# Kernel optimization log

Measured on AMD Instinct MI355X. Metric: run time of the kernel, lower is better.

## Reference

```python
import jax, jax.numpy as jnp
import numpy as np

N_QUBITS = 8
N_WORDS = 16
DEGREE = 3
N_ANSATZ_LAYERS = 2
VOCAB = 50257
EMB = 512
BATCH = 16
N_ROTS = 4 * N_QUBITS * N_ANSATZ_LAYERS  # 64
DIM = 2 ** N_QUBITS


def _ry_mat(th):
    # [[cos, -sin],[sin, cos]] on theta/2, batched over leading dim
    c = jnp.cos(th / 2).astype(jnp.complex64)
    s = jnp.sin(th / 2).astype(jnp.complex64)
    return jnp.stack([jnp.stack([c, -s], -1), jnp.stack([s, c], -1)], -2)


def _rx_mat(th):
    # [[cos, -i sin],[-i sin, cos]] on theta/2
    c = jnp.cos(th / 2).astype(jnp.complex64)
    s = jnp.sin(th / 2).astype(jnp.complex64)
    return jnp.stack([jnp.stack([c, -1j * s], -1), jnp.stack([-1j * s, c], -1)], -2)


def _apply_1q(st, M, w):
    # st: [BB, 2^n] complex, M: [BB,2,2]; wire 0 is the most-significant axis (tq convention)
    BB = st.shape[0]
    s = st.reshape(BB, 2 ** w, 2, -1)
    s = jnp.einsum('bij,bljr->blir', M, s)
    return s.reshape(BB, -1)


def _apply_ctrl(st, M, c, t, n):
    # controlled-1q gate: apply M on target t only in the control=1 subspace
    BB = st.shape[0]
    full = st.reshape((BB,) + (2,) * n)
    s0 = jnp.take(full, 0, axis=c + 1)
    s1 = jnp.take(full, 1, axis=c + 1)
    ta = (t if t < c else t - 1) + 1  # target axis after removing control axis
    s1 = jnp.moveaxis(s1, ta, -1)
    s1 = jnp.einsum('bij,b...j->b...i', M, s1)
    s1 = jnp.moveaxis(s1, -1, ta)
    return jnp.stack([s0, s1], axis=c + 1).reshape(BB, -1)


def _sim14(st, params, n, layers):
    # circuit-14 ansatz: ry ring, crx down-ring, ry ring, crx up-ring (per layer)
    idx = 0
    for _ in range(layers):
        for i in range(n):
            st = _apply_1q(st, _ry_mat(params[:, idx]), i); idx += 1
        for i in range(n - 1, -1, -1):
            st = _apply_ctrl(st, _rx_mat(params[:, idx]), i, (i + 1) % n, n); idx += 1
        for i in range(n):
            st = _apply_1q(st, _ry_mat(params[:, idx]), i); idx += 1
        for i in [n - 1] + list(range(n - 1)):
            st = _apply_ctrl(st, _rx_mat(params[:, idx]), i, (i - 1) % n, n); idx += 1
    return st


def _apply_unitaries(base, wparams, coeffs):
    # base: [B, DIM]; wparams: [B, W, N_ROTS]; coeffs: [B, W] complex -> LCU sum_w c_w U_w |psi>
    B, W = wparams.shape[0], wparams.shape[1]
    rep = jnp.repeat(base, W, axis=0)  # matches torch repeat(1,W).view(-1,DIM)
    st = _sim14(rep, wparams.reshape(B * W, -1), N_QUBITS, N_ANSATZ_LAYERS)
    return jnp.einsum('bwi,bw->bi', st.reshape(B, W, DIM), coeffs)


def _measure_xyz(st, n):
    # Pauli X/Y/Z expectations per wire; order: [x_0..x_{n-1}, y_..., z_...]
    BB = st.shape[0]
    xs, ys, zs = [], [], []
    for w in range(n):
        s = st.reshape(BB, 2 ** w, 2, -1)
        a0, a1 = s[:, :, 0, :], s[:, :, 1, :]
        cross = jnp.sum(jnp.conj(a0) * a1, axis=(1, 2))
        xs.append(2 * jnp.real(cross))
        ys.append(2 * jnp.imag(cross))
        zs.append(jnp.sum(jnp.abs(a0) ** 2 - jnp.abs(a1) ** 2, axis=(1, 2)))
    return jnp.concatenate([jnp.stack(xs, -1), jnp.stack(ys, -1), jnp.stack(zs, -1)], axis=-1)


def reference(x, embedding_W, emb2rot_W, emb2rot_b, poly_coeffs, mix_coeffs_ri, qff_params, ff1_W, ff1_b, ff2_W, ff2_b):
    B = x.shape[0]
    mix = (mix_coeffs_ri[:, 0] + 1j * mix_coeffs_ri[:, 1]).astype(jnp.complex64)
    coeffs = mix / jnp.maximum(jnp.sum(jnp.abs(mix)), 1e-12)  # L1 normalize
    coeffs = jnp.broadcast_to(coeffs[None, :], (B, N_WORDS))
    emb = embedding_W[x]                       # [B, W, EMB]
    wparams = emb @ emb2rot_W.T + emb2rot_b    # [B, W, N_ROTS]; dropout is identity in eval
    base = jnp.zeros((B, DIM), jnp.complex64).at[:, 0].set(1.0)
    acc = poly_coeffs[0] * base
    work = base
    for d in range(1, DEGREE + 1):
        work = _apply_unitaries(work, wparams, coeffs)
        acc = acc + poly_coeffs[d] * work
    mixed = acc / jnp.sum(jnp.abs(poly_coeffs))
    final_probs = jnp.linalg.norm(mixed, axis=-1)
    normed = mixed / jnp.maximum(final_probs, 1e-12)[:, None]
    qp = jnp.broadcast_to(qff_params[None, :4 * N_QUBITS], (B, 4 * N_QUBITS))  # qff uses 1 layer
    st = _sim14(normed, qp, N_QUBITS, 1)
    exps = _measure_xyz(st, N_QUBITS)          # [B, 3*n_qubits]
    h = jax.nn.relu(exps @ ff1_W.T + ff1_b)
    op = h @ ff2_W.T + ff2_b
    return op, jnp.mean(final_probs)


def setup_inputs():
    key = jax.random.key(0)
    ks = jax.random.split(key, 12)
    x = jax.random.randint(ks[0], (BATCH, N_WORDS), 0, VOCAB)
    embedding_W = jax.random.normal(ks[1], (VOCAB, EMB), jnp.float32) * 0.02
    emb2rot_W = jax.random.normal(ks[2], (N_ROTS, EMB), jnp.float32) * (1.0 / np.sqrt(EMB))
    emb2rot_b = jax.random.normal(ks[3], (N_ROTS,), jnp.float32) * 0.01
    poly_coeffs = jax.random.uniform(ks[4], (DEGREE + 1,), jnp.float32)
    mix_coeffs_ri = jax.random.uniform(ks[5], (N_WORDS, 2), jnp.float32)
    qff_params = jax.random.uniform(ks[6], (N_ROTS,), jnp.float32)
    NM = 3 * N_QUBITS
    ff1_W = jax.random.normal(ks[7], (EMB, NM), jnp.float32) * (1.0 / np.sqrt(NM))
    ff1_b = jnp.zeros((EMB,), jnp.float32)
    ff2_W = jax.random.normal(ks[8], (VOCAB, EMB), jnp.float32) * (1.0 / np.sqrt(EMB))
    ff2_b = jnp.zeros((VOCAB,), jnp.float32)
    return {"x": x, "embedding_W": embedding_W, "emb2rot_W": emb2rot_W, "emb2rot_b": emb2rot_b,
            "poly_coeffs": poly_coeffs, "mix_coeffs_ri": mix_coeffs_ri, "qff_params": qff_params,
            "ff1_W": ff1_W, "ff1_b": ff1_b, "ff2_W": ff2_W, "ff2_b": ff2_b}
```

## Files before the change

### kernel.cpp

```cpp
#include <hip/hip_runtime.h>
#include <hip/hip_bf16.h>

#define NQ 8
#define DIM 256
#define NB 16
#define NW 16
#define VOCABN 50257
#define EMBN 512

__device__ __forceinline__ float2 shfl2(float2 a, int m){
  float2 r; r.x = __shfl_xor(a.x, m, 64); r.y = __shfl_xor(a.y, m, 64); return r;
}
__device__ __forceinline__ float wave_sum(float x){
  #pragma unroll
  for (int off = 1; off < 64; off <<= 1) x += __shfl_xor(x, off, 64);
  return x;
}

__device__ __forceinline__ void ry_pair(float2& a0, float2& a1, float c, float s){
  float2 n0 = make_float2(c*a0.x - s*a1.x, c*a0.y - s*a1.y);
  float2 n1 = make_float2(s*a0.x + c*a1.x, s*a0.y + c*a1.y);
  a0 = n0; a1 = n1;
}
__device__ __forceinline__ void rx_pair(float2& a0, float2& a1, float c, float s){
  float2 n0 = make_float2(c*a0.x + s*a1.y, c*a0.y - s*a1.x);
  float2 n1 = make_float2(c*a1.x + s*a0.y, c*a1.y - s*a0.x);
  a0 = n0; a1 = n1;
}

__device__ __forceinline__ void apply_gate(float2 v[4], int lane, int kind, int cbit, int tbit,
                                           float c, float s){
  if (kind == 0){
    if (tbit == 7){ ry_pair(v[0], v[2], c, s); ry_pair(v[1], v[3], c, s); }
    else if (tbit == 6){ ry_pair(v[0], v[1], c, s); ry_pair(v[2], v[3], c, s); }
    else {
      int m = 1 << tbit;
      #pragma unroll
      for (int r = 0; r < 4; ++r){
        float2 w = shfl2(v[r], m);
        float sg = (lane & m) ? s : -s;
        v[r] = make_float2(c*v[r].x + sg*w.x, c*v[r].y + sg*w.y);
      }
    }
  } else {
    if (tbit >= 6){
      if (cbit >= 6){
        if (cbit == 7) rx_pair(v[2], v[3], c, s);
        else           rx_pair(v[1], v[3], c, s);
      } else {
        int cm = 1 << cbit;
        if (lane & cm){
          if (tbit == 7){ rx_pair(v[0], v[2], c, s); rx_pair(v[1], v[3], c, s); }
          else          { rx_pair(v[0], v[1], c, s); rx_pair(v[2], v[3], c, s); }
        }
      }
    } else {
      int m = 1 << tbit;
      if (cbit >= 6){
        int r0 = (cbit == 6) ? 1 : 2;
        float2 w0 = shfl2(v[r0], m);
        float2 w1 = shfl2(v[3], m);
        v[r0] = make_float2(c*v[r0].x + s*w0.y, c*v[r0].y - s*w0.x);
        v[3]  = make_float2(c*v[3].x  + s*w1.y, c*v[3].y  - s*w1.x);
      } else {
        int cm = 1 << cbit;
        bool act = (lane & cm) != 0;
        #pragma unroll
        for (int r = 0; r < 4; ++r){
          float2 w = shfl2(v[r], m);
          if (act) v[r] = make_float2(c*v[r].x + s*w.y, c*v[r].y - s*w.x);
        }
      }
    }
  }
}

__device__ __forceinline__ void sim32(float2 v[4], int lane, const float2* __restrict__ cs){
  constexpr int KIND[32] = {0,0,0,0,0,0,0,0, 1,1,1,1,1,1,1,1, 0,0,0,0,0,0,0,0, 1,1,1,1,1,1,1,1};
  constexpr int CB[32]   = {0,0,0,0,0,0,0,0, 0,1,2,3,4,5,6,7, 0,0,0,0,0,0,0,0, 0,7,6,5,4,3,2,1};
  constexpr int TB[32]   = {7,6,5,4,3,2,1,0, 7,0,1,2,3,4,5,6, 7,6,5,4,3,2,1,0, 1,0,7,6,5,4,3,2};
  #pragma unroll
  for (int g = 0; g < 32; ++g){
    float2 p = cs[g];
    apply_gate(v, lane, KIND[g], CB[g], TB[g], p.x, p.y);
  }
}

__device__ __forceinline__ void measure_xyz(const float2 v[4], int lane, float* exps){
  #pragma unroll
  for (int q = 0; q < 8; ++q){
    const int t = 7 - q;
    float xr = 0.f, xi = 0.f, zz = 0.f;
    if (t == 7){
      #pragma unroll
      for (int r = 0; r < 2; ++r){
        float2 a0 = v[r], a1 = v[r+2];
        xr += a0.x*a1.x + a0.y*a1.y;
        xi += a0.x*a1.y - a0.y*a1.x;
        zz += (a0.x*a0.x + a0.y*a0.y) - (a1.x*a1.x + a1.y*a1.y);
      }
    } else if (t == 6){
      #pragma unroll
      for (int r = 0; r < 4; r += 2){
        float2 a0 = v[r], a1 = v[r+1];
        xr += a0.x*a1.x + a0.y*a1.y;
        xi += a0.x*a1.y - a0.y*a1.x;
        zz += (a0.x*a0.x + a0.y*a0.y) - (a1.x*a1.x + a1.y*a1.y);
      }
    } else {
      int m = 1 << t;
      #pragma unroll
      for (int r = 0; r < 4; ++r){
        float2 a = v[r];
        float2 w = shfl2(a, m);
        if (!(lane & m)){
          xr += a.x*w.x + a.y*w.y;
          xi += a.x*w.y - a.y*w.x;
          zz += (a.x*a.x + a.y*a.y) - (w.x*w.x + w.y*w.y);
        }
      }
    }
    xr = wave_sum(xr); xi = wave_sum(xi); zz = wave_sum(zz);
    if (lane == 0){ exps[q] = 2.f*xr; exps[8+q] = 2.f*xi; exps[16+q] = zz; }
  }
}

__global__ __launch_bounds__(64) void k_prep(
    const int* __restrict__ x, const float* __restrict__ embW,
    const float* __restrict__ e2rW, const float* __restrict__ e2rb,
    const float* __restrict__ mixri, const float* __restrict__ qff,
    float* __restrict__ wcs, float* __restrict__ coeffs, float* __restrict__ qcs)
{
  const int p = blockIdx.x;
  const int j = threadIdx.x;
  const int tok = x[p];
  const float4* er = (const float4*)(embW + (size_t)tok * EMBN);
  const float4* wr = (const float4*)(e2rW + (size_t)j * EMBN);
  float acc = e2rb[j];
  #pragma unroll 4
  for (int k = 0; k < EMBN/4; ++k){
    float4 e = er[k], w4 = wr[k];
    acc += e.x*w4.x + e.y*w4.y + e.z*w4.z + e.w*w4.w;
  }
  float th = 0.5f * acc;
  wcs[(p*64 + j)*2 + 0] = cosf(th);
  wcs[(p*64 + j)*2 + 1] = sinf(th);
  if (p == 0){
    if (j < 32){ float t = 0.5f * qff[j]; qcs[2*j] = cosf(t); qcs[2*j+1] = sinf(t); }
    if (j < 16){
      float ssum = 0.f;
      for (int i = 0; i < 16; ++i){
        float mr = mixri[2*i], mi = mixri[2*i+1];
        ssum += sqrtf(mr*mr + mi*mi);
      }
      ssum = fmaxf(ssum, 1e-12f);
      coeffs[2*j]   = mixri[2*j]   / ssum;
      coeffs[2*j+1] = mixri[2*j+1] / ssum;
    }
  }
}

__global__ __launch_bounds__(1024) void k_sim(
    const float* __restrict__ wcs, const float* __restrict__ coeffs,
    const float* __restrict__ qcs, const float* __restrict__ poly,
    const float* __restrict__ ff1W, const float* __restrict__ ff1b,
    float* __restrict__ hT, float* __restrict__ fprobs)
{
  const int b = blockIdx.x;
  const int tid = threadIdx.x;
  const int w = tid >> 6;
  const int lane = tid & 63;

  __shared__ float2 stall[NW][DIM];
  __shared__ float2 partial[4][DIM];
  __shared__ float2 work[DIM];
  __shared__ float2 accs[DIM];
  __shared__ float exps[24];

  if (tid < DIM){
    float p0 = poly[0];
    float one = (tid == 0) ? 1.f : 0.f;
    work[tid] = make_float2(one, 0.f);
    accs[tid] = make_float2(p0*one, 0.f);
  }
  __syncthreads();

  const float2 coef = make_float2(coeffs[2*w], coeffs[2*w+1]);
  const float2* mycs = ((const float2*)wcs) + (b*NW + w)*64;

  for (int d = 1; d <= 3; ++d){
    float2 v[4];
    #pragma unroll
    for (int r = 0; r < 4; ++r) v[r] = work[(r<<6) | lane];
    for (int l = 0; l < 2; ++l) sim32(v, lane, mycs + 32*l);
    #pragma unroll
    for (int r = 0; r < 4; ++r){
      float2 a = v[r];
      stall[w][(r<<6) | lane] = make_float2(coef.x*a.x - coef.y*a.y, coef.x*a.y + coef.y*a.x);
    }
    __syncthreads();
    {
      int idx = tid & 255, grp = tid >> 8;
      float2 s = make_float2(0.f, 0.f);
      #pragma unroll
      for (int ww = 0; ww < 4; ++ww){
        float2 a = stall[grp*4 + ww][idx];
        s.x += a.x; s.y += a.y;
      }
      partial[grp][idx] = s;
    }
    __syncthreads();
    if (tid < DIM){
      float2 s = make_float2(0.f, 0.f);
      #pragma unroll
      for (int g2 = 0; g2 < 4; ++g2){ s.x += partial[g2][tid].x; s.y += partial[g2][tid].y; }
      float pd = poly[d];
      work[tid] = s;
      accs[tid].x += pd*s.x; accs[tid].y += pd*s.y;
    }
    __syncthreads();
  }

  const float psum = fabsf(poly[0]) + fabsf(poly[1]) + fabsf(poly[2]) + fabsf(poly[3]);
  if (tid < DIM){
    work[tid] = make_float2(accs[tid].x/psum, accs[tid].y/psum);
  }
  __syncthreads();

  if (w == 0){
    float2 v[4];
    float ss = 0.f;
    #pragma unroll
    for (int r = 0; r < 4; ++r){
      float2 m = work[(r<<6) | lane];
      v[r] = m; ss += m.x*m.x + m.y*m.y;
    }
    ss = wave_sum(ss);
    float fp = sqrtf(ss);
    if (lane == 0) fprobs[b] = fp;
    float inv = 1.f / fmaxf(fp, 1e-12f);
    #pragma unroll
    for (int r = 0; r < 4; ++r){ v[r].x *= inv; v[r].y *= inv; }
    sim32(v, lane, (const float2*)qcs);
    measure_xyz(v, lane, exps);
  }
  __syncthreads();

  if (tid < EMBN){
    float a = ff1b[tid];
    const float* wr = ff1W + tid*24;
    #pragma unroll
    for (int m2 = 0; m2 < 24; ++m2) a += exps[m2]*wr[m2];
    a = fmaxf(a, 0.f);
    hT[tid*NB + b] = a;
  }
}

__global__ __launch_bounds__(256) void k_out(
    const float* __restrict__ hT, const float* __restrict__ ff2W,
    const float* __restrict__ ff2b, const float* __restrict__ fprobs,
    float* __restrict__ out)
{
  const int v = blockIdx.x*256 + threadIdx.x;
  if (blockIdx.x == 0 && threadIdx.x == 0){
    float s = 0.f;
    #pragma unroll
    for (int i = 0; i < 16; ++i) s += fprobs[i];
    out[(size_t)NB*VOCABN] = s * (1.f/16.f);
  }
  if (v >= VOCABN) return;
  const float4* wr = (const float4*)(ff2W + (size_t)v * EMBN);
  float acc[16];
  #pragma unroll
  for (int i = 0; i < 16; ++i) acc[i] = 0.f;
  for (int kc = 0; kc < EMBN/4; ++kc){
    float4 w4 = wr[kc];
    const float* hk = hT + kc*64;
    #pragma unroll
    for (int i = 0; i < 16; ++i)
      acc[i] += w4.x*hk[i] + w4.y*hk[16+i] + w4.z*hk[32+i] + w4.w*hk[48+i];
  }
  float bias = ff2b[v];
  #pragma unroll
  for (int i = 0; i < 16; ++i) out[(size_t)i*VOCABN + v] = acc[i] + bias;
}

extern "C" void kernel_launch(void* const* d_in, const int* in_sizes, int n_in,
                              void* d_out, int out_size, void* d_ws, size_t ws_size,
                              hipStream_t stream)
{
  const int*   x     = (const int*)  d_in[0];
  const float* embW  = (const float*)d_in[1];
  const float* e2rW  = (const float*)d_in[2];
  const float* e2rb  = (const float*)d_in[3];
  const float* poly  = (const float*)d_in[4];
  const float* mixri = (const float*)d_in[5];
  const float* qff   = (const float*)d_in[6];
  const float* ff1W  = (const float*)d_in[7];
  const float* ff1b  = (const float*)d_in[8];
  const float* ff2W  = (const float*)d_in[9];
  const float* ff2b  = (const float*)d_in[10];
  float* out = (float*)d_out;
  float* ws  = (float*)d_ws;

  float* wcs    = ws;
  float* coeffs = ws + 32768;
  float* qcs    = ws + 32800;
  float* hT     = ws + 32864;
  float* fprobs = ws + 41056;

  k_prep<<<256, 64, 0, stream>>>(x, embW, e2rW, e2rb, mixri, qff, wcs, coeffs, qcs);
  k_sim <<<NB, 1024, 0, stream>>>(wcs, coeffs, qcs, poly, ff1W, ff1b, hT, fprobs);
  k_out <<<(VOCABN + 255)/256, 256, 0, stream>>>(hT, ff2W, ff2b, fprobs, out);
}
```

Baseline: 319.2 us.

## Fuse prep into sim kernel and stage hidden states in LDS for output GEMV

Folds the embedding-to-rotation prep kernel into the simulation kernel, so each wave computes its own cos/sin angles into shared memory and one launch plus its global round trip disappear. The output projection now copies the whole hidden matrix into shared memory and gives each row to two threads, each covering half of K. The halves are combined through shared memory. This trades global/L2 reads of hT for LDS reads and doubles the thread count per row, while the fused prep runs on only 16 blocks.

```diff
diff --git a/kernel.cpp b/kernel.cpp
--- a/kernel.cpp
+++ b/kernel.cpp
@@ -125,44 +125,11 @@
   }
 }
 
-__global__ __launch_bounds__(64) void k_prep(
+__global__ __launch_bounds__(1024) void k_sim(
     const int* __restrict__ x, const float* __restrict__ embW,
     const float* __restrict__ e2rW, const float* __restrict__ e2rb,
     const float* __restrict__ mixri, const float* __restrict__ qff,
-    float* __restrict__ wcs, float* __restrict__ coeffs, float* __restrict__ qcs)
-{
-  const int p = blockIdx.x;
-  const int j = threadIdx.x;
-  const int tok = x[p];
-  const float4* er = (const float4*)(embW + (size_t)tok * EMBN);
-  const float4* wr = (const float4*)(e2rW + (size_t)j * EMBN);
-  float acc = e2rb[j];
-  #pragma unroll 4
-  for (int k = 0; k < EMBN/4; ++k){
-    float4 e = er[k], w4 = wr[k];
-    acc += e.x*w4.x + e.y*w4.y + e.z*w4.z + e.w*w4.w;
-  }
-  float th = 0.5f * acc;
-  wcs[(p*64 + j)*2 + 0] = cosf(th);
-  wcs[(p*64 + j)*2 + 1] = sinf(th);
-  if (p == 0){
-    if (j < 32){ float t = 0.5f * qff[j]; qcs[2*j] = cosf(t); qcs[2*j+1] = sinf(t); }
-    if (j < 16){
-      float ssum = 0.f;
-      for (int i = 0; i < 16; ++i){
-        float mr = mixri[2*i], mi = mixri[2*i+1];
-        ssum += sqrtf(mr*mr + mi*mi);
-      }
-      ssum = fmaxf(ssum, 1e-12f);
-      coeffs[2*j]   = mixri[2*j]   / ssum;
-      coeffs[2*j+1] = mixri[2*j+1] / ssum;
-    }
-  }
-}
-
-__global__ __launch_bounds__(1024) void k_sim(
-    const float* __restrict__ wcs, const float* __restrict__ coeffs,
-    const float* __restrict__ qcs, const float* __restrict__ poly,
+    const float* __restrict__ poly,
     const float* __restrict__ ff1W, const float* __restrict__ ff1b,
     float* __restrict__ hT, float* __restrict__ fprobs)
 {
@@ -171,22 +138,50 @@
   const int w = tid >> 6;
   const int lane = tid & 63;
 
+  __shared__ float2 wcs_s[NW][64];
+  __shared__ float2 qcs_s[32];
+  __shared__ float  ssum_s;
   __shared__ float2 stall[NW][DIM];
   __shared__ float2 partial[4][DIM];
   __shared__ float2 work[DIM];
   __shared__ float2 accs[DIM];
   __shared__ float exps[24];
 
-  if (tid < DIM){
-    float p0 = poly[0];
-    float one = (tid == 0) ? 1.f : 0.f;
-    work[tid] = make_float2(one, 0.f);
-    accs[tid] = make_float2(p0*one, 0.f);
-  }
-  __syncthreads();
-
-  const float2 coef = make_float2(coeffs[2*w], coeffs[2*w+1]);
-  const float2* mycs = ((const float2*)wcs) + (b*NW + w)*64;
+  {
+    const int j = lane;
+    const int tok = x[b*NW + w];
+    const float4* er  = (const float4*)(embW + (size_t)tok * EMBN);
+    const float4* wr4 = (const float4*)(e2rW + (size_t)j * EMBN);
+    float acc = e2rb[j];
+    #pragma unroll 4
+    for (int k = 0; k < EMBN/4; ++k){
+      float4 e = er[k], w4 = wr4[k];
+      acc += e.x*w4.x + e.y*w4.y + e.z*w4.z + e.w*w4.w;
+    }
+    float th = 0.5f * acc;
+    wcs_s[w][j] = make_float2(cosf(th), sinf(th));
+    if (tid < 32){ float t = 0.5f * qff[tid]; qcs_s[tid] = make_float2(cosf(t), sinf(t)); }
+    if (tid == 0){
+      float ssum = 0.f;
+      #pragma unroll
+      for (int i = 0; i < 16; ++i){
+        float mr = mixri[2*i], mi = mixri[2*i+1];
+        ssum += sqrtf(mr*mr + mi*mi);
+      }
+      ssum_s = fmaxf(ssum, 1e-12f);
+    }
+    if (tid < DIM){
+      float p0 = poly[0];
+      float one = (tid == 0) ? 1.f : 0.f;
+      work[tid] = make_float2(one, 0.f);
+      accs[tid] = make_float2(p0*one, 0.f);
+    }
+  }
+  __syncthreads();
+
+  const float inv_ssum = 1.f / ssum_s;
+  const float2 coef = make_float2(mixri[2*w]*inv_ssum, mixri[2*w+1]*inv_ssum);
+  const float2* mycs = &wcs_s[w][0];
 
   for (int d = 1; d <= 3; ++d){
     float2 v[4];
@@ -241,7 +236,7 @@
     float inv = 1.f / fmaxf(fp, 1e-12f);
     #pragma unroll
     for (int r = 0; r < 4; ++r){ v[r].x *= inv; v[r].y *= inv; }
-    sim32(v, lane, (const float2*)qcs);
+    sim32(v, lane, &qcs_s[0]);
     measure_xyz(v, lane, exps);
   }
   __syncthreads();
@@ -261,28 +256,93 @@
     const float* __restrict__ ff2b, const float* __restrict__ fprobs,
     float* __restrict__ out)
 {
-  const int v = blockIdx.x*256 + threadIdx.x;
-  if (blockIdx.x == 0 && threadIdx.x == 0){
+  __shared__ float4 smem[2048];
+  const int tid = threadIdx.x;
+
+  if (blockIdx.x == 0 && tid == 0){
     float s = 0.f;
     #pragma unroll
     for (int i = 0; i < 16; ++i) s += fprobs[i];
     out[(size_t)NB*VOCABN] = s * (1.f/16.f);
   }
-  if (v >= VOCABN) return;
-  const float4* wr = (const float4*)(ff2W + (size_t)v * EMBN);
-  float acc[16];
-  #pragma unroll
-  for (int i = 0; i < 16; ++i) acc[i] = 0.f;
-  for (int kc = 0; kc < EMBN/4; ++kc){
-    float4 w4 = wr[kc];
-    const float* hk = hT + kc*64;
-    #pragma unroll
-    for (int i = 0; i < 16; ++i)
-      acc[i] += w4.x*hk[i] + w4.y*hk[16+i] + w4.z*hk[32+i] + w4.w*hk[48+i];
-  }
-  float bias = ff2b[v];
-  #pragma unroll
-  for (int i = 0; i < 16; ++i) out[(size_t)i*VOCABN + v] = acc[i] + bias;
+
+  {
+    const float4* hT4 = (const float4*)hT;
+    #pragma unroll
+    for (int i = 0; i < 8; ++i) smem[i*256 + tid] = hT4[i*256 + tid];
+  }
+  __syncthreads();
+
+  const int rrow = tid & 127;
+  const int half = tid >> 7;
+  const int row  = blockIdx.x * 128 + rrow;
+  const bool valid = (row < VOCABN);
+
+  float4 a0 = make_float4(0,0,0,0), a1 = a0, a2 = a0, a3 = a0;
+
+  if (valid){
+    const float4* wv = (const float4*)(ff2W + (size_t)row * EMBN) + half*64;
+    const int kbase = half*256;
+    #pragma unroll 8
+    for (int c = 0; c < 64; ++c){
+      float4 wq = wv[c];
+      const int k0 = (kbase + c*4) << 2;
+      float4 h00 = smem[k0+0],  h01 = smem[k0+1],  h02 = smem[k0+2],  h03 = smem[k0+3];
+      float4 h10 = smem[k0+4],  h11 = smem[k0+5],  h12 = smem[k0+6],  h13 = smem[k0+7];
+      float4 h20 = smem[k0+8],  h21 = smem[k0+9],  h22 = smem[k0+10], h23 = smem[k0+11];
+      float4 h30 = smem[k0+12], h31 = smem[k0+13], h32 = smem[k0+14], h33 = smem[k0+15];
+      a0.x += wq.x*h00.x + wq.y*h10.x + wq.z*h20.x + wq.w*h30.x;
+      a0.y += wq.x*h00.y + wq.y*h10.y + wq.z*h20.y + wq.w*h30.y;
+      a0.z += wq.x*h00.z + wq.y*h10.z + wq.z*h20.z + wq.w*h30.z;
+      a0.w += wq.x*h00.w + wq.y*h10.w + wq.z*h20.w + wq.w*h30.w;
+      a1.x += wq.x*h01.x + wq.y*h11.x + wq.z*h21.x + wq.w*h31.x;
+      a1.y += wq.x*h01.y + wq.y*h11.y + wq.z*h21.y + wq.w*h31.y;
+      a1.z += wq.x*h01.z + wq.y*h11.z + wq.z*h21.z + wq.w*h31.z;
+      a1.w += wq.x*h01.w + wq.y*h11.w + wq.z*h21.w + wq.w*h31.w;
+      a2.x += wq.x*h02.x + wq.y*h12.x + wq.z*h22.x + wq.w*h32.x;
+      a2.y += wq.x*h02.y + wq.y*h12.y + wq.z*h22.y + wq.w*h32.y;
+      a2.z += wq.x*h02.z + wq.y*h12.z + wq.z*h22.z + wq.w*h32.z;
+      a2.w += wq.x*h02.w + wq.y*h12.w + wq.z*h22.w + wq.w*h32.w;
+      a3.x += wq.x*h03.x + wq.y*h13.x + wq.z*h23.x + wq.w*h33.x;
+      a3.y += wq.x*h03.y + wq.y*h13.y + wq.z*h23.y + wq.w*h33.y;
+      a3.z += wq.x*h03.z + wq.y*h13.z + wq.z*h23.z + wq.w*h33.z;
+      a3.w += wq.x*h03.w + wq.y*h13.w + wq.z*h23.w + wq.w*h33.w;
+    }
+  }
+  __syncthreads();
+
+  if (half == 1){
+    smem[0*128 + rrow] = a0;
+    smem[1*128 + rrow] = a1;
+    smem[2*128 + rrow] = a2;
+    smem[3*128 + rrow] = a3;
+  }
+  __syncthreads();
+  if (half == 0 && valid){
+    float4 b0 = smem[0*128 + rrow], b1 = smem[1*128 + rrow];
+    float4 b2 = smem[2*128 + rrow], b3 = smem[3*128 + rrow];
+    a0.x += b0.x; a0.y += b0.y; a0.z += b0.z; a0.w += b0.w;
+    a1.x += b1.x; a1.y += b1.y; a1.z += b1.z; a1.w += b1.w;
+    a2.x += b2.x; a2.y += b2.y; a2.z += b2.z; a2.w += b2.w;
+    a3.x += b3.x; a3.y += b3.y; a3.z += b3.z; a3.w += b3.w;
+    const float bias = ff2b[row];
+    out[(size_t) 0*VOCABN + row] = a0.x + bias;
+    out[(size_t) 1*VOCABN + row] = a0.y + bias;
+    out[(size_t) 2*VOCABN + row] = a0.z + bias;
+    out[(size_t) 3*VOCABN + row] = a0.w + bias;
+    out[(size_t) 4*VOCABN + row] = a1.x + bias;
+    out[(size_t) 5*VOCABN + row] = a1.y + bias;
+    out[(size_t) 6*VOCABN + row] = a1.z + bias;
+    out[(size_t) 7*VOCABN + row] = a1.w + bias;
+    out[(size_t) 8*VOCABN + row] = a2.x + bias;
+    out[(size_t) 9*VOCABN + row] = a2.y + bias;
+    out[(size_t)10*VOCABN + row] = a2.z + bias;
+    out[(size_t)11*VOCABN + row] = a2.w + bias;
+    out[(size_t)12*VOCABN + row] = a3.x + bias;
+    out[(size_t)13*VOCABN + row] = a3.y + bias;
+    out[(size_t)14*VOCABN + row] = a3.z + bias;
+    out[(size_t)15*VOCABN + row] = a3.w + bias;
+  }
 }
 
 extern "C" void kernel_launch(void* const* d_in, const int* in_sizes, int n_in,
@@ -303,13 +363,9 @@
   float* out = (float*)d_out;
   float* ws  = (float*)d_ws;
 
-  float* wcs    = ws;
-  float* coeffs = ws + 32768;
-  float* qcs    = ws + 32800;
-  float* hT     = ws + 32864;
-  float* fprobs = ws + 41056;
-
-  k_prep<<<256, 64, 0, stream>>>(x, embW, e2rW, e2rb, mixri, qff, wcs, coeffs, qcs);
-  k_sim <<<NB, 1024, 0, stream>>>(wcs, coeffs, qcs, poly, ff1W, ff1b, hT, fprobs);
-  k_out <<<(VOCABN + 255)/256, 256, 0, stream>>>(hT, ff2W, ff2b, fprobs, out);
-}
+  float* hT     = ws;
+  float* fprobs = ws + 8192;
+
+  k_sim<<<NB, 1024, 0, stream>>>(x, embW, e2rW, e2rb, mixri, qff, poly, ff1W, ff1b, hT, fprobs);
+  k_out<<<(VOCABN + 127)/128, 256, 0, stream>>>(hT, ff2W, ff2b, fprobs, out);
+}
```

Result: slower. 356.2 us (+11.6%).
